# Kernel optimization log

Measured on AMD Instinct MI355X. Metric: run time of the kernel, lower is better.

The kernel has to match this reference:

```python
import jax, jax.numpy as jnp
import numpy as np

N, E, G, F_IN = 50000, 200000, 2000, 373
NEG_SLOPE, BN_EPS = 0.2, 1e-5


def _bn(x, g, b, m, v):
    # BatchNorm1d in eval mode with running stats
    return (x - m) * jax.lax.rsqrt(v + BN_EPS) * g + b


def _gcn(x, src, dst, w, b):
    # PyG GCNConv: add self loops, sym-normalize D^-1/2 (A+I) D^-1/2, then aggregate.
    n = x.shape[0]
    h = x @ w  # [N, out]
    deg = jax.ops.segment_sum(jnp.ones_like(src, jnp.float32), dst, n) + 1.0  # +1 self loop
    dinv = jax.lax.rsqrt(deg)
    agg = jax.ops.segment_sum((dinv[src] * dinv[dst])[:, None] * h[src], dst, n)
    # self-loop contribution has norm dinv[i]^2
    return agg + (dinv * dinv)[:, None] * h + b


def _gat(x, src, dst, w, a_s, a_d, b, H, C):
    # PyG GATConv (concat=True): per-edge attention logits, segment softmax over
    # incoming edges (incl. self loop, handled analytically), scatter-add aggregate.
    n = x.shape[0]
    h = (x @ w).reshape(n, H, C)  # [N, H, C]
    al_s = jnp.einsum('nhc,hc->nh', h, a_s)  # source-side logit term
    al_d = jnp.einsum('nhc,hc->nh', h, a_d)  # dest-side logit term
    e = jax.nn.leaky_relu(al_s[src] + al_d[dst], NEG_SLOPE)  # [E, H]
    e_self = jax.nn.leaky_relu(al_s + al_d, NEG_SLOPE)       # [N, H] self-loop logit
    m = jnp.maximum(jax.ops.segment_max(e, dst, n), e_self)  # stable softmax max
    we = jnp.exp(e - m[dst])
    ws = jnp.exp(e_self - m)
    denom = jax.ops.segment_sum(we, dst, n) + ws
    out = jax.ops.segment_sum(we[:, :, None] * h[src], dst, n) + ws[:, :, None] * h
    return (out / denom[:, :, None]).reshape(n, H * C) + b


def _forward(fl, edge_index, batch):
    (x, gw1, gb1, gw2, gb2, gw3, gb3,
     g01g, g01b, g01m, g01v, g02g, g02b, g02m, g02v, g03g, g03b, g03m, g03v,
     aw1, as1, ad1, ab1, aw2, as2, ad2, ab2, aw3, as3, ad3, ab3,
     g11g, g11b, g11m, g11v, g12g, g12b, g12m, g12v, g13g, g13b, g13m, g13v,
     f1w, f1b, f2w, f2b, f3w, f3b) = fl
    src, dst = edge_index[0], edge_index[1]
    xg = _bn(jax.nn.relu(_gcn(x, src, dst, gw1, gb1)), g01g, g01b, g01m, g01v)
    xg = _bn(jax.nn.relu(_gcn(xg, src, dst, gw2, gb2)), g02g, g02b, g02m, g02v)
    xg = _bn(jax.nn.relu(_gcn(xg, src, dst, gw3, gb3)), g03g, g03b, g03m, g03v)
    xg = jax.ops.segment_sum(xg, batch, G)  # global_add_pool -> [G, 128]
    y = _bn(jax.nn.relu(_gat(x, src, dst, aw1, as1, ad1, ab1, 3, 256)), g11g, g11b, g11m, g11v)
    y = _bn(jax.nn.relu(_gat(y, src, dst, aw2, as2, ad2, ab2, 3, 128)), g12g, g12b, g12m, g12v)
    y = _bn(jax.nn.relu(_gat(y, src, dst, aw3, as3, ad3, ab3, 3, 128)), g13g, g13b, g13m, g13v)
    y = jax.ops.segment_sum(y, batch, G)  # [G, 384]
    cr = jnp.concatenate([xg, y], axis=1)  # [G, 512]
    cr = jax.nn.relu(cr @ f1w + f1b)  # dropout is identity in eval mode
    cr = jax.nn.relu(cr @ f2w + f2b)
    cr = jax.nn.relu(cr @ f3w + f3b)
    return cr.reshape(-1)  # [G]


def setup_inputs() -> dict:
    key = jax.random.key(0)
    keys = jax.random.split(key, 80)
    ki = iter(range(80))
    def nrm(shape, s=0.05):
        return jax.random.normal(keys[next(ki)], shape, jnp.float32) * s
    inp = {}
    inp['x'] = jax.random.normal(keys[next(ki)], (N, F_IN), jnp.float32)
    inp['edge_index'] = jax.random.randint(keys[next(ki)], (2, E), 0, N, dtype=jnp.int32)
    inp['batch'] = jnp.sort(jax.random.randint(keys[next(ki)], (N,), 0, G, dtype=jnp.int32))
    for i, o, t in [(373, 256, '1'), (256, 128, '2'), (128, 128, '3')]:
        inp['gw' + t] = nrm((i, o))
        inp['gb' + t] = jnp.zeros((o,), jnp.float32)
    for t, d in [('01', 256), ('02', 128), ('03', 128), ('11', 768), ('12', 384), ('13', 384)]:
        inp['g' + t + 'g'] = jnp.ones((d,), jnp.float32)
        inp['g' + t + 'b'] = jnp.zeros((d,), jnp.float32)
        inp['g' + t + 'm'] = nrm((d,))
        inp['g' + t + 'v'] = jax.random.uniform(keys[next(ki)], (d,), jnp.float32) + 0.5
    for i, o, t in [(373, 256, '1'), (768, 128, '2'), (384, 128, '3')]:
        inp['aw' + t] = nrm((i, 3 * o))
        inp['as' + t] = nrm((3, o))
        inp['ad' + t] = nrm((3, o))
        inp['ab' + t] = jnp.zeros((3 * o,), jnp.float32)
    for i, o, t in [(512, 256, '1'), (256, 64, '2'), (64, 1, '3')]:
        inp['f' + t + 'w'] = nrm((i, o))
        inp['f' + t + 'b'] = jnp.zeros((o,), jnp.float32)
    return inp


def reference(x, gw1, gb1, gw2, gb2, gw3, gb3,
              g01g, g01b, g01m, g01v, g02g, g02b, g02m, g02v, g03g, g03b, g03m, g03v,
              aw1, as1, ad1, ab1, aw2, as2, ad2, ab2, aw3, as3, ad3, ab3,
              g11g, g11b, g11m, g11v, g12g, g12b, g12m, g12v, g13g, g13b, g13m, g13v,
              f1w, f1b, f2w, f2b, f3w, f3b, edge_index, batch):
    fl = (x, gw1, gb1, gw2, gb2, gw3, gb3,
          g01g, g01b, g01m, g01v, g02g, g02b, g02m, g02v, g03g, g03b, g03m, g03v,
          aw1, as1, ad1, ab1, aw2, as2, ad2, ab2, aw3, as3, ad3, ab3,
          g11g, g11b, g11m, g11v, g12g, g12b, g12m, g12v, g13g, g13b, g13m, g13v,
          f1w, f1b, f2w, f2b, f3w, f3b)
    return _forward(fl, edge_index, batch)
```

## Files before the change

### kernel.cpp

```cpp
#include <hip/hip_runtime.h>
#include <cstdint>
#include <cstddef>

#define N_NODES 50000
#define N_EDGES 200000
#define N_GRAPHS 2000
#define F_IN 373
#define NEG_SLOPE 0.2f
#define BN_EPS 1e-5f

typedef float f32x4 __attribute__((ext_vector_type(4)));
typedef float f32x2 __attribute__((ext_vector_type(2)));
typedef short s16x8 __attribute__((ext_vector_type(8)));
typedef short s16x4 __attribute__((ext_vector_type(4)));
typedef unsigned int u32x4 __attribute__((ext_vector_type(4)));

template <int VPT> struct VecT;
template <> struct VecT<2> { using type = f32x2; };
template <> struct VecT<4> { using type = f32x4; };

static inline int cdiv(long long a, long long b) { return (int)((a + b - 1) / b); }

__device__ __forceinline__ float lrelu(float x) { return x > 0.f ? x : NEG_SLOPE * x; }

__device__ __forceinline__ void atomAddF(float* p, float v) {
#if defined(__HIP_DEVICE_COMPILE__)
  unsafeAtomicAdd(p, v);
#else
  atomicAdd(p, v);
#endif
}

__device__ __forceinline__ unsigned short bf16rne(float f) {
  unsigned u = __float_as_uint(f);
  unsigned r = u + 0x7fffu + ((u >> 16) & 1u);
  return (unsigned short)(r >> 16);
}
__device__ __forceinline__ void split2(float f, unsigned short& hi, unsigned short& lo) {
  hi = bf16rne(f);
  float fh = __uint_as_float(((unsigned)hi) << 16);
  lo = bf16rne(f - fh);
}
__device__ __forceinline__ unsigned packsplit(float f) {
  unsigned short hi, lo;
  split2(f, hi, lo);
  return (((unsigned)hi) << 16) | (unsigned)lo;
}

__device__ __forceinline__ int swz(int row, int k) {
  return ((row >> 4) << 9) | ((k >> 3) << 7) | ((((row & 15) ^ (k >> 3))) << 3) | (k & 7);
}

__global__ void k_zero(float* p, long long n) {
  long long i = (long long)blockIdx.x * blockDim.x + threadIdx.x;
  if (i < n) p[i] = 0.f;
}
__global__ void k_zero_i(int* p, int n) {
  int i = blockIdx.x * blockDim.x + threadIdx.x;
  if (i < n) p[i] = 0;
}
__global__ void k_deg(int* __restrict__ deg, const int* __restrict__ dst, int e) {
  int i = blockIdx.x * blockDim.x + threadIdx.x;
  if (i < e) atomicAdd(&deg[dst[i]], 1);
}
__global__ void k_dinv(const int* __restrict__ deg, float* __restrict__ dinv, int n) {
  int i = blockIdx.x * blockDim.x + threadIdx.x;
  if (i < n) dinv[i] = rsqrtf((float)deg[i] + 1.0f);
}

__global__ void k_scan(const int* __restrict__ deg, int* __restrict__ rowptr,
                       int* __restrict__ cursor, int n) {
  __shared__ int wsum[16];
  __shared__ int carry_s;
  const int lane = threadIdx.x & 63;
  const int wid = threadIdx.x >> 6;
  if (threadIdx.x == 0) carry_s = 0;
  __syncthreads();
  for (int base = 0; base < n; base += 1024) {
    int i = base + threadIdx.x;
    int v = (i < n) ? deg[i] : 0;
    int s = v;
#pragma unroll
    for (int off = 1; off < 64; off <<= 1) {
      int t = __shfl_up(s, off);
      if (lane >= off) s += t;
    }
    if (lane == 63) wsum[wid] = s;
    __syncthreads();
    if (threadIdx.x == 0) {
      int acc = carry_s;
#pragma unroll
      for (int w = 0; w < 16; w++) { int t = wsum[w]; wsum[w] = acc; acc += t; }
      carry_s = acc;
    }
    __syncthreads();
    if (i < n) { rowptr[i] = wsum[wid] + s - v; cursor[i] = 0; }
    __syncthreads();
  }
  if (threadIdx.x == 0) rowptr[n] = carry_s;
}

__global__ void k_csr_scatter(const int* __restrict__ src, const int* __restrict__ dst,
                              const int* __restrict__ rowptr, int* __restrict__ cursor,
                              int* __restrict__ csr_src, int e) {
  int i = blockIdx.x * blockDim.x + threadIdx.x;
  if (i >= e) return;
  int d = dst[i];
  int pos = rowptr[d] + atomicAdd(&cursor[d], 1);
  csr_src[pos] = src[i];
}

__global__ void k_buildwt(const float* __restrict__ W, int ldW, int col0, int Nsub,
                          int K, int Kpad, unsigned* __restrict__ Wt) {
  int n = blockIdx.x * blockDim.x + threadIdx.x;
  int k = blockIdx.y;
  if (n >= Nsub) return;
  float v = (k < K) ? W[(size_t)k * ldW + col0 + n] : 0.f;
  Wt[(size_t)n * Kpad + k] = packsplit(v);
}

__global__ __launch_bounds__(256) void k_mfma_gemm(
    const float* __restrict__ Ap, int lda, int amode, int Kact,
    const unsigned* __restrict__ Wt, int Kpad,
    float* __restrict__ C, int M, int ldC, int col0,
    const float* __restrict__ a_s, const float* __restrict__ a_d,
    float* __restrict__ als, float* __restrict__ ald, int lshift) {
  __shared__ unsigned short Ah[64 * 32], Al[64 * 32], Bh[128 * 32], Bl[128 * 32];
  const int bm = blockIdx.y * 64;
  const int bn = blockIdx.x * 128;
  const int tid = threadIdx.x;
  const int lane = tid & 63;
  const int wave = tid >> 6;
  const int wm = wave & 1;
  const int wn = wave >> 1;

  f32x4 acc[2][4];
#pragma unroll
  for (int i = 0; i < 2; i++)
#pragma unroll
    for (int j = 0; j < 4; j++) acc[i][j] = (f32x4){0.f, 0.f, 0.f, 0.f};

  const int srow = tid >> 3;
  const int skq = (tid & 7) << 2;

  for (int k0 = 0; k0 < Kpad; k0 += 32) {
#pragma unroll
    for (int i = 0; i < 2; i++) {
      int row = i * 32 + srow;
      int grow = bm + row;
      unsigned short hv[4], lv[4];
      if (amode == 2) {
        f32x4 v = (grow < M) ? *(const f32x4*)(Ap + (size_t)grow * lda + k0 + skq)
                             : (f32x4){0.f, 0.f, 0.f, 0.f};
#pragma unroll
        for (int u = 0; u < 4; u++) split2(v[u], hv[u], lv[u]);
      } else {
        const float* ap = Ap + (size_t)grow * lda;
#pragma unroll
        for (int u = 0; u < 4; u++) {
          int kc = k0 + skq + u;
          float f = (grow < M && kc < Kact) ? ap[kc] : 0.f;
          split2(f, hv[u], lv[u]);
        }
      }
      int eb = swz(row, skq);
      *(s16x4*)&Ah[eb] = *(s16x4*)hv;
      *(s16x4*)&Al[eb] = *(s16x4*)lv;
    }
#pragma unroll
    for (int i = 0; i < 4; i++) {
      int row = i * 32 + srow;
      u32x4 v = *(const u32x4*)(Wt + (size_t)(bn + row) * Kpad + k0 + skq);
      unsigned short hv[4], lv[4];
#pragma unroll
      for (int u = 0; u < 4; u++) { hv[u] = (unsigned short)(v[u] >> 16); lv[u] = (unsigned short)(v[u] & 0xffffu); }
      int eb = swz(row, skq);
      *(s16x4*)&Bh[eb] = *(s16x4*)hv;
      *(s16x4*)&Bl[eb] = *(s16x4*)lv;
    }
    __syncthreads();
    const int koct = lane >> 4;
    const int mrow = lane & 15;
    const int fo = (koct << 7) + (((mrow ^ koct)) << 3);
    s16x8 ah[2], al[2];
#pragma unroll
    for (int g = 0; g < 2; g++) {
      int ab = ((wm * 2 + g) << 9) + fo;
      ah[g] = *(const s16x8*)&Ah[ab];
      al[g] = *(const s16x8*)&Al[ab];
    }
#pragma unroll
    for (int j = 0; j < 4; j++) {
      int bb = ((wn * 4 + j) << 9) + fo;
      s16x8 bhj = *(const s16x8*)&Bh[bb];
      s16x8 blj = *(const s16x8*)&Bl[bb];
#pragma unroll
      for (int g = 0; g < 2; g++) {
        acc[g][j] = __builtin_amdgcn_mfma_f32_16x16x32_bf16(ah[g], bhj, acc[g][j], 0, 0, 0);
        acc[g][j] = __builtin_amdgcn_mfma_f32_16x16x32_bf16(al[g], bhj, acc[g][j], 0, 0, 0);
        acc[g][j] = __builtin_amdgcn_mfma_f32_16x16x32_bf16(ah[g], blj, acc[g][j], 0, 0, 0);
      }
    }
    __syncthreads();
  }
  const int mrow = lane & 15;
  const int rq = (lane >> 4) << 2;
  float asv[4], adv[4];
  if (a_s) {
#pragma unroll
    for (int j = 0; j < 4; j++) {
      int c = bn + wn * 64 + j * 16 + mrow;
      asv[j] = a_s[c];
      adv[j] = a_d[c];
    }
  }
  const int head = bn >> lshift;
#pragma unroll
  for (int g = 0; g < 2; g++) {
#pragma unroll
    for (int r = 0; r < 4; r++) {
      int row = bm + wm * 32 + g * 16 + rq + r;
      bool rok = row < M;
      float ps = 0.f, pd = 0.f;
#pragma unroll
      for (int j = 0; j < 4; j++) {
        int ccol = bn + wn * 64 + j * 16 + mrow;
        float v = acc[g][j][r];
        if (rok) C[(size_t)row * ldC + col0 + ccol] = v;
        ps += v * asv[j];
        pd += v * adv[j];
      }
      if (a_s) {
#pragma unroll
        for (int off = 1; off < 16; off <<= 1) {
          ps += __shfl_xor(ps, off);
          pd += __shfl_xor(pd, off);
        }
        if (mrow == 0 && rok) {
          atomAddF(&als[(size_t)head * N_NODES + row], ps);
          atomAddF(&ald[(size_t)head * N_NODES + row], pd);
        }
      }
    }
  }
}

__global__ __launch_bounds__(256) void k_gemm(
    const float* __restrict__ A, const float* __restrict__ W,
    const float* __restrict__ bias, float* __restrict__ C,
    int M, int K, int Nsub, int ldW, int ldC, int col0, int flags) {
  __shared__ float As[16][68];
  __shared__ float Bs[16][68];
  const int bm = blockIdx.y * 64;
  const int bn = blockIdx.x * 64;
  const int tid = threadIdx.x;
  const int tm = (tid >> 4) << 2;
  const int tn = (tid & 15) << 2;
  float acc[4][4] = {};
  for (int k0 = 0; k0 < K; k0 += 16) {
    {
      int idx = tid * 4;
      int row = idx >> 4;
      int kk = idx & 15;
      const float* ap = A + (size_t)(bm + row) * K + k0 + kk;
      bool rok = (bm + row) < M;
#pragma unroll
      for (int i = 0; i < 4; i++) {
        int kcur = k0 + kk + i;
        As[kk + i][row] = (rok && kcur < K) ? ap[i] : 0.f;
      }
    }
#pragma unroll
    for (int i = 0; i < 4; i++) {
      int idx = tid + i * 256;
      int kk = idx >> 6;
      int nn = idx & 63;
      int kcur = k0 + kk;
      Bs[kk][nn] = (kcur < K && (bn + nn) < Nsub)
                       ? W[(size_t)kcur * ldW + col0 + bn + nn] : 0.f;
    }
    __syncthreads();
#pragma unroll
    for (int kk = 0; kk < 16; kk++) {
      float av[4], bv[4];
#pragma unroll
      for (int i = 0; i < 4; i++) av[i] = As[kk][tm + i];
#pragma unroll
      for (int j = 0; j < 4; j++) bv[j] = Bs[kk][tn + j];
#pragma unroll
      for (int i = 0; i < 4; i++)
#pragma unroll
        for (int j = 0; j < 4; j++) acc[i][j] += av[i] * bv[j];
    }
    __syncthreads();
  }
#pragma unroll
  for (int i = 0; i < 4; i++) {
    int row = bm + tm + i;
    if (row >= M) continue;
#pragma unroll
    for (int j = 0; j < 4; j++) {
      int col = bn + tn + j;
      if (col >= Nsub) continue;
      float v = acc[i][j];
      if (flags & 1) v += bias[col0 + col];
      if (flags & 2) v = fmaxf(v, 0.f);
      C[(size_t)row * ldC + col] = v;
    }
  }
}

template <int VPT>
__global__ __launch_bounds__(256) void k_gcn_fused(
    const float* __restrict__ h, const float* __restrict__ dinv,
    const int* __restrict__ rowptr, const int* __restrict__ csr_src,
    const float* __restrict__ bias, const float* __restrict__ g,
    const float* __restrict__ b, const float* __restrict__ m,
    const float* __restrict__ vv, float* __restrict__ out, int n, int F) {
  using V = typename VecT<VPT>::type;
  int wid = (blockIdx.x * blockDim.x + threadIdx.x) >> 6;
  int lane = threadIdx.x & 63;
  if (wid >= n) return;
  const int fo = lane * VPT;
  float dd = dinv[wid];
  V acc = *(const V*)(h + (size_t)wid * F + fo) * (dd * dd) + *(const V*)(bias + fo);
  int e0 = rowptr[wid], e1 = rowptr[wid + 1];
  for (int e = e0; e < e1; e++) {
    int s = csr_src[e];
    float w = dinv[s] * dd;
    acc += *(const V*)(h + (size_t)s * F + fo) * w;
  }
  V mg = *(const V*)(m + fo);
  V vg = *(const V*)(vv + fo);
  V gg = *(const V*)(g + fo);
  V bg = *(const V*)(b + fo);
  V res;
#pragma unroll
  for (int u = 0; u < VPT; u++) {
    float val = fmaxf(acc[u], 0.f);
    res[u] = (val - mg[u]) * rsqrtf(vg[u] + BN_EPS) * gg[u] + bg[u];
  }
  *(V*)(out + (size_t)wid * F + fo) = res;
}

template <int VPT>
__global__ __launch_bounds__(256) void k_gat_fused(
    const float* __restrict__ h, int ldH,
    const float* __restrict__ als, const float* __restrict__ ald,
    const int* __restrict__ rowptr, const int* __restrict__ csr_src,
    const float* __restrict__ bias, const float* __restrict__ g,
    const float* __restrict__ b, const float* __restrict__ m,
    const float* __restrict__ vv, float* __restrict__ out, int ldO, int col0, int n) {
  using V = typename VecT<VPT>::type;
  int wid = (blockIdx.x * blockDim.x + threadIdx.x) >> 6;
  int lane = threadIdx.x & 63;
  if (wid >= n) return;
  const int co = lane * VPT;
  float aldd = ald[wid];
  float self_lg = lrelu(als[wid] + aldd);
  int e0 = rowptr[wid], e1 = rowptr[wid + 1];
  float mx = self_lg;
  for (int e = e0; e < e1; e++) {
    mx = fmaxf(mx, lrelu(als[csr_src[e]] + aldd));
  }
  float den = __expf(self_lg - mx);
  V acc = *(const V*)(h + (size_t)wid * ldH + co) * den;
  for (int e = e0; e < e1; e++) {
    int s = csr_src[e];
    float w = __expf(lrelu(als[s] + aldd) - mx);
    den += w;
    acc += *(const V*)(h + (size_t)s * ldH + co) * w;
  }
  float rden = 1.f / den;
  const int fo = col0 + co;
  V bi = *(const V*)(bias + fo);
  V mg = *(const V*)(m + fo);
  V vg = *(const V*)(vv + fo);
  V gg = *(const V*)(g + fo);
  V bg = *(const V*)(b + fo);
  V res;
#pragma unroll
  for (int u = 0; u < VPT; u++) {
    float val = fmaxf(acc[u] * rden + bi[u], 0.f);
    res[u] = (val - mg[u]) * rsqrtf(vg[u] + BN_EPS) * gg[u] + bg[u];
  }
  *(V*)(out + (size_t)wid * ldO + fo) = res;
}

__global__ void k_pool_add(float* __restrict__ pooled, const float* __restrict__ act,
                           const int* __restrict__ batch, int n, int F, int off) {
  long long idx = (long long)blockIdx.x * blockDim.x + threadIdx.x;
  if (idx >= (long long)n * F) return;
  int node = (int)(idx / F);
  int f = (int)(idx % F);
  atomAddF(&pooled[(size_t)batch[node] * 512 + off + f], act[idx]);
}
__global__ void k_fc3(const float* __restrict__ in, const float* __restrict__ w,
                      const float* __restrict__ b, float* __restrict__ out, int g) {
  int wid = (blockIdx.x * blockDim.x + threadIdx.x) >> 6;
  int lane = threadIdx.x & 63;
  if (wid >= g) return;
  float v = in[wid * 64 + lane] * w[lane];
#pragma unroll
  for (int off = 32; off > 0; off >>= 1) v += __shfl_down(v, off);
  if (lane == 0) out[wid] = fmaxf(v + b[0], 0.f);
}

static void gemm_fp32(hipStream_t s, const float* A, const float* W, const float* bias,
                      float* C, int M, int K, int Nsub, int ldW, int ldC, int col0, int flags) {
  dim3 grid(cdiv(Nsub, 64), cdiv(M, 64));
  k_gemm<<<grid, 256, 0, s>>>(A, W, bias, C, M, K, Nsub, ldW, ldC, col0, flags);
}

static void gemm_mfma(hipStream_t s, const float* A, int lda, int amode,
                      const float* W, int ldW, int wcol0, int K, int Kpad,
                      unsigned* Wt, float* C, int M, int Nsub, int ldC, int ccol0,
                      const float* a_s = nullptr, const float* a_d = nullptr,
                      float* als = nullptr, float* ald = nullptr, int lshift = 30) {
  dim3 wg(cdiv(Nsub, 256), Kpad);
  k_buildwt<<<wg, 256, 0, s>>>(W, ldW, wcol0, Nsub, K, Kpad, Wt);
  dim3 grid(Nsub / 128, cdiv(M, 64));
  k_mfma_gemm<<<grid, 256, 0, s>>>(A, lda, amode, K, Wt, Kpad, C, M, ldC, ccol0,
                                   a_s, a_d, als, ald, lshift);
}

extern "C" void kernel_launch(void* const* d_in, const int* in_sizes, int n_in,
                              void* d_out, int out_size, void* d_ws, size_t ws_size,
                              hipStream_t stream) {
  const float* x = (const float*)d_in[0];
  const int* ei = (const int*)d_in[1];
  const int* batch = (const int*)d_in[2];
  const float* gw1 = (const float*)d_in[3];  const float* gb1 = (const float*)d_in[4];
  const float* gw2 = (const float*)d_in[5];  const float* gb2 = (const float*)d_in[6];
  const float* gw3 = (const float*)d_in[7];  const float* gb3 = (const float*)d_in[8];
  const float* g01g = (const float*)d_in[9];  const float* g01b = (const float*)d_in[10];
  const float* g01m = (const float*)d_in[11]; const float* g01v = (const float*)d_in[12];
  const float* g02g = (const float*)d_in[13]; const float* g02b = (const float*)d_in[14];
  const float* g02m = (const float*)d_in[15]; const float* g02v = (const float*)d_in[16];
  const float* g03g = (const float*)d_in[17]; const float* g03b = (const float*)d_in[18];
  const float* g03m = (const float*)d_in[19]; const float* g03v = (const float*)d_in[20];
  const float* g11g = (const float*)d_in[21]; const float* g11b = (const float*)d_in[22];
  const float* g11m = (const float*)d_in[23]; const float* g11v = (const float*)d_in[24];
  const float* g12g = (const float*)d_in[25]; const float* g12b = (const float*)d_in[26];
  const float* g12m = (const float*)d_in[27]; const float* g12v = (const float*)d_in[28];
  const float* g13g = (const float*)d_in[29]; const float* g13b = (const float*)d_in[30];
  const float* g13m = (const float*)d_in[31]; const float* g13v = (const float*)d_in[32];
  const float* aw1 = (const float*)d_in[33]; const float* as1 = (const float*)d_in[34];
  const float* ad1 = (const float*)d_in[35]; const float* ab1 = (const float*)d_in[36];
  const float* aw2 = (const float*)d_in[37]; const float* as2 = (const float*)d_in[38];
  const float* ad2 = (const float*)d_in[39]; const float* ad2b = nullptr;
  const float* ab2 = (const float*)d_in[40];
  const float* aw3 = (const float*)d_in[41]; const float* as3 = (const float*)d_in[42];
  const float* ad3 = (const float*)d_in[43]; const float* ab3 = (const float*)d_in[44];
  const float* f1w = (const float*)d_in[45]; const float* f1b = (const float*)d_in[46];
  const float* f2w = (const float*)d_in[47]; const float* f2b = (const float*)d_in[48];
  const float* f3w = (const float*)d_in[49]; const float* f3b = (const float*)d_in[50];
  (void)ad2b;

  const int* src = ei;
  const int* dst = ei + N_EDGES;

  size_t need = 0;
  need += (size_t)N_NODES * 768;
  need += (size_t)N_NODES * 384;
  need += (size_t)N_NODES;
  need += (size_t)N_NODES * 6;
  need += (size_t)N_NODES + 1;
  need += (size_t)N_EDGES;
  need += (size_t)N_GRAPHS * (512 + 256 + 64);
  if (ws_size < need * sizeof(float)) return;

  float* wp = (float*)d_ws;
  float* OUT = wp;     wp += (size_t)N_NODES * 768;
  float* H = wp;       wp += (size_t)N_NODES * 384;
  float* dinv = wp;    wp += N_NODES;
  float* als3 = wp;    wp += (size_t)N_NODES * 3;
  float* ald3 = wp;    wp += (size_t)N_NODES * 3;
  int* rowptr = (int*)wp;  wp += N_NODES + 1;
  int* csr_src = (int*)wp; wp += N_EDGES;
  float* pooled = wp; wp += (size_t)N_GRAPHS * 512;
  float* fc1 = wp;    wp += (size_t)N_GRAPHS * 256;
  float* fc2 = wp;    wp += (size_t)N_GRAPHS * 64;
  int* degi = (int*)als3;
  int* cursor = (int*)ald3;
  unsigned* Wt = (unsigned*)fc1;

  k_zero_i<<<cdiv(N_NODES, 256), 256, 0, stream>>>(degi, N_NODES);
  k_deg<<<cdiv(N_EDGES, 256), 256, 0, stream>>>(degi, dst, N_EDGES);
  k_dinv<<<cdiv(N_NODES, 256), 256, 0, stream>>>(degi, dinv, N_NODES);
  k_scan<<<1, 1024, 0, stream>>>(degi, rowptr, cursor, N_NODES);
  k_csr_scatter<<<cdiv(N_EDGES, 256), 256, 0, stream>>>(src, dst, rowptr, cursor, csr_src, N_EDGES);
  k_zero<<<cdiv((long long)N_GRAPHS * 512, 256), 256, 0, stream>>>(pooled, (long long)N_GRAPHS * 512);

  const int nodeWaveGrid = cdiv((long long)N_NODES * 64, 256);

  struct { const float *w, *bias, *g, *b, *m, *v; int F; } gcn[3] = {
    {gw1, gb1, g01g, g01b, g01m, g01v, 256},
    {gw2, gb2, g02g, g02b, g02m, g02v, 128},
    {gw3, gb3, g03g, g03b, g03m, g03v, 128}};
  int gF = F_IN;
  for (int l = 0; l < 3; l++) {
    int F = gcn[l].F;
    if (l == 0)
      gemm_mfma(stream, x, F_IN, 0, gcn[l].w, F, 0, F_IN, 384, Wt, H, N_NODES, F, F, 0);
    else
      gemm_mfma(stream, OUT, gF, 2, gcn[l].w, F, 0, gF, gF, Wt, H, N_NODES, F, F, 0);
    if (F == 256)
      k_gcn_fused<4><<<nodeWaveGrid, 256, 0, stream>>>(H, dinv, rowptr, csr_src,
          gcn[l].bias, gcn[l].g, gcn[l].b, gcn[l].m, gcn[l].v, OUT, N_NODES, F);
    else
      k_gcn_fused<2><<<nodeWaveGrid, 256, 0, stream>>>(H, dinv, rowptr, csr_src,
          gcn[l].bias, gcn[l].g, gcn[l].b, gcn[l].m, gcn[l].v, OUT, N_NODES, F);
    gF = F;
  }
  k_pool_add<<<cdiv((long long)N_NODES * 128, 256), 256, 0, stream>>>(pooled, OUT, batch, N_NODES, 128, 0);

  {
    int C = 256, HC = 768;
    for (int hh = 0; hh < 3; hh++) {
      k_zero<<<cdiv((long long)N_NODES * 6, 256), 256, 0, stream>>>(als3, (long long)N_NODES * 6);
      gemm_mfma(stream, x, F_IN, 0, aw1, HC, hh * C, F_IN, 384, Wt, H, N_NODES, C, C, 0,
                as1 + hh * C, ad1 + hh * C, als3, ald3, 30);
      k_gat_fused<4><<<nodeWaveGrid, 256, 0, stream>>>(H, C, als3, ald3, rowptr, csr_src,
          ab1, g11g, g11b, g11m, g11v, OUT, HC, hh * C, N_NODES);
    }
  }

  struct { const float *w, *s, *d, *bias, *g, *b, *m, *v; int K; } gat[2] = {
    {aw2, as2, ad2, ab2, g12g, g12b, g12m, g12v, 768},
    {aw3, as3, ad3, ab3, g13g, g13b, g13m, g13v, 384}};
  for (int l = 0; l < 2; l++) {
    int C = 128, HC = 384;
    k_zero<<<cdiv((long long)N_NODES * 6, 256), 256, 0, stream>>>(als3, (long long)N_NODES * 6);
    gemm_mfma(stream, OUT, gat[l].K, 2, gat[l].w, HC, 0, gat[l].K, gat[l].K, Wt, H, N_NODES, HC, HC, 0,
              gat[l].s, gat[l].d, als3, ald3, 7);
    for (int hh = 0; hh < 3; hh++) {
      k_gat_fused<2><<<nodeWaveGrid, 256, 0, stream>>>(H + hh * C, HC,
          als3 + (size_t)hh * N_NODES, ald3 + (size_t)hh * N_NODES, rowptr, csr_src,
          gat[l].bias, gat[l].g, gat[l].b, gat[l].m, gat[l].v, OUT, HC, hh * C, N_NODES);
    }
  }
  k_pool_add<<<cdiv((long long)N_NODES * 384, 256), 256, 0, stream>>>(pooled, OUT, batch, N_NODES, 384, 128);

  gemm_fp32(stream, pooled, f1w, f1b, fc1, N_GRAPHS, 512, 256, 256, 256, 0, 3);
  gemm_fp32(stream, fc1, f2w, f2b, fc2, N_GRAPHS, 256, 64, 64, 64, 0, 3);
  k_fc3<<<cdiv((long long)N_GRAPHS * 64, 256), 256, 0, stream>>>(fc2, f3w, f3b, (float*)d_out, N_GRAPHS);
}
```

Before: 1.732 ms.

## Store activations as packed bf16 hi/lo pairs and pad GEMM LDS segments

The GCN and GAT aggregation kernels now write their outputs pre-split into packed bf16 hi/lo words, so the downstream MFMA GEMM loads them with a new amode that only unpacks bits instead of redoing the float split. Pooling unpacks those words back to float. The LDS tile layout also changes from an XOR swizzle to padded 136-element segments to avoid bank conflicts. The aim is to take split arithmetic out of the GEMM A-tile load, at the cost of a small precision change in pooling and extra LDS footprint.

```diff
diff --git a/kernel.cpp b/kernel.cpp
--- a/kernel.cpp
+++ b/kernel.cpp
@@ -14,10 +14,14 @@
 typedef short s16x8 __attribute__((ext_vector_type(8)));
 typedef short s16x4 __attribute__((ext_vector_type(4)));
 typedef unsigned int u32x4 __attribute__((ext_vector_type(4)));
+typedef unsigned int u32x2 __attribute__((ext_vector_type(2)));
 
 template <int VPT> struct VecT;
 template <> struct VecT<2> { using type = f32x2; };
 template <> struct VecT<4> { using type = f32x4; };
+template <int VPT> struct UVecT;
+template <> struct UVecT<2> { using type = u32x2; };
+template <> struct UVecT<4> { using type = u32x4; };
 
 static inline int cdiv(long long a, long long b) { return (int)((a + b - 1) / b); }
 
@@ -46,9 +50,13 @@
   split2(f, hi, lo);
   return (((unsigned)hi) << 16) | (unsigned)lo;
 }
-
-__device__ __forceinline__ int swz(int row, int k) {
-  return ((row >> 4) << 9) | ((k >> 3) << 7) | ((((row & 15) ^ (k >> 3))) << 3) | (k & 7);
+__device__ __forceinline__ float unpackf(unsigned w) {
+  return __uint_as_float(w & 0xffff0000u) + __uint_as_float(w << 16);
+}
+
+#define SEGSZ 136
+__device__ __forceinline__ int ebase(int row, int k) {
+  return ((row >> 4) * 4 + (k >> 3)) * SEGSZ + ((row & 15) << 3) + (k & 7);
 }
 
 __global__ void k_zero(float* p, long long n) {
@@ -125,7 +133,8 @@
     float* __restrict__ C, int M, int ldC, int col0,
     const float* __restrict__ a_s, const float* __restrict__ a_d,
     float* __restrict__ als, float* __restrict__ ald, int lshift) {
-  __shared__ unsigned short Ah[64 * 32], Al[64 * 32], Bh[128 * 32], Bl[128 * 32];
+  __shared__ unsigned short Ah[16 * SEGSZ], Al[16 * SEGSZ];
+  __shared__ unsigned short Bh[32 * SEGSZ], Bl[32 * SEGSZ];
   const int bm = blockIdx.y * 64;
   const int bn = blockIdx.x * 128;
   const int tid = threadIdx.x;
@@ -149,7 +158,12 @@
       int row = i * 32 + srow;
       int grow = bm + row;
       unsigned short hv[4], lv[4];
-      if (amode == 2) {
+      if (amode == 1) {
+        u32x4 v = (grow < M) ? *(const u32x4*)((const unsigned*)Ap + (size_t)grow * lda + k0 + skq)
+                             : (u32x4){0u, 0u, 0u, 0u};
+#pragma unroll
+        for (int u = 0; u < 4; u++) { hv[u] = (unsigned short)(v[u] >> 16); lv[u] = (unsigned short)(v[u] & 0xffffu); }
+      } else if (amode == 2) {
         f32x4 v = (grow < M) ? *(const f32x4*)(Ap + (size_t)grow * lda + k0 + skq)
                              : (f32x4){0.f, 0.f, 0.f, 0.f};
 #pragma unroll
@@ -163,7 +177,7 @@
           split2(f, hv[u], lv[u]);
         }
       }
-      int eb = swz(row, skq);
+      int eb = ebase(row, skq);
       *(s16x4*)&Ah[eb] = *(s16x4*)hv;
       *(s16x4*)&Al[eb] = *(s16x4*)lv;
     }
@@ -174,24 +188,23 @@
       unsigned short hv[4], lv[4];
 #pragma unroll
       for (int u = 0; u < 4; u++) { hv[u] = (unsigned short)(v[u] >> 16); lv[u] = (unsigned short)(v[u] & 0xffffu); }
-      int eb = swz(row, skq);
+      int eb = ebase(row, skq);
       *(s16x4*)&Bh[eb] = *(s16x4*)hv;
       *(s16x4*)&Bl[eb] = *(s16x4*)lv;
     }
     __syncthreads();
     const int koct = lane >> 4;
     const int mrow = lane & 15;
-    const int fo = (koct << 7) + (((mrow ^ koct)) << 3);
     s16x8 ah[2], al[2];
 #pragma unroll
     for (int g = 0; g < 2; g++) {
-      int ab = ((wm * 2 + g) << 9) + fo;
+      int ab = ((wm * 2 + g) * 4 + koct) * SEGSZ + (mrow << 3);
       ah[g] = *(const s16x8*)&Ah[ab];
       al[g] = *(const s16x8*)&Al[ab];
     }
 #pragma unroll
     for (int j = 0; j < 4; j++) {
-      int bb = ((wn * 4 + j) << 9) + fo;
+      int bb = ((wn * 4 + j) * 4 + koct) * SEGSZ + (mrow << 3);
       s16x8 bhj = *(const s16x8*)&Bh[bb];
       s16x8 blj = *(const s16x8*)&Bl[bb];
 #pragma unroll
@@ -316,8 +329,9 @@
     const int* __restrict__ rowptr, const int* __restrict__ csr_src,
     const float* __restrict__ bias, const float* __restrict__ g,
     const float* __restrict__ b, const float* __restrict__ m,
-    const float* __restrict__ vv, float* __restrict__ out, int n, int F) {
+    const float* __restrict__ vv, unsigned* __restrict__ out, int n, int F) {
   using V = typename VecT<VPT>::type;
+  using UV = typename UVecT<VPT>::type;
   int wid = (blockIdx.x * blockDim.x + threadIdx.x) >> 6;
   int lane = threadIdx.x & 63;
   if (wid >= n) return;
@@ -334,13 +348,13 @@
   V vg = *(const V*)(vv + fo);
   V gg = *(const V*)(g + fo);
   V bg = *(const V*)(b + fo);
-  V res;
+  UV res;
 #pragma unroll
   for (int u = 0; u < VPT; u++) {
     float val = fmaxf(acc[u], 0.f);
-    res[u] = (val - mg[u]) * rsqrtf(vg[u] + BN_EPS) * gg[u] + bg[u];
-  }
-  *(V*)(out + (size_t)wid * F + fo) = res;
+    res[u] = packsplit((val - mg[u]) * rsqrtf(vg[u] + BN_EPS) * gg[u] + bg[u]);
+  }
+  *(UV*)(out + (size_t)wid * F + fo) = res;
 }
 
 template <int VPT>
@@ -350,8 +364,9 @@
     const int* __restrict__ rowptr, const int* __restrict__ csr_src,
     const float* __restrict__ bias, const float* __restrict__ g,
     const float* __restrict__ b, const float* __restrict__ m,
-    const float* __restrict__ vv, float* __restrict__ out, int ldO, int col0, int n) {
+    const float* __restrict__ vv, unsigned* __restrict__ out, int ldO, int col0, int n) {
   using V = typename VecT<VPT>::type;
+  using UV = typename UVecT<VPT>::type;
   int wid = (blockIdx.x * blockDim.x + threadIdx.x) >> 6;
   int lane = threadIdx.x & 63;
   if (wid >= n) return;
@@ -378,22 +393,22 @@
   V vg = *(const V*)(vv + fo);
   V gg = *(const V*)(g + fo);
   V bg = *(const V*)(b + fo);
-  V res;
+  UV res;
 #pragma unroll
   for (int u = 0; u < VPT; u++) {
     float val = fmaxf(acc[u] * rden + bi[u], 0.f);
-    res[u] = (val - mg[u]) * rsqrtf(vg[u] + BN_EPS) * gg[u] + bg[u];
-  }
-  *(V*)(out + (size_t)wid * ldO + fo) = res;
-}
-
-__global__ void k_pool_add(float* __restrict__ pooled, const float* __restrict__ act,
+    res[u] = packsplit((val - mg[u]) * rsqrtf(vg[u] + BN_EPS) * gg[u] + bg[u]);
+  }
+  *(UV*)(out + (size_t)wid * ldO + fo) = res;
+}
+
+__global__ void k_pool_add(float* __restrict__ pooled, const unsigned* __restrict__ act,
                            const int* __restrict__ batch, int n, int F, int off) {
   long long idx = (long long)blockIdx.x * blockDim.x + threadIdx.x;
   if (idx >= (long long)n * F) return;
   int node = (int)(idx / F);
   int f = (int)(idx % F);
-  atomAddF(&pooled[(size_t)batch[node] * 512 + off + f], act[idx]);
+  atomAddF(&pooled[(size_t)batch[node] * 512 + off + f], unpackf(act[idx]));
 }
 __global__ void k_fc3(const float* __restrict__ in, const float* __restrict__ w,
                       const float* __restrict__ b, float* __restrict__ out, int g) {
@@ -412,7 +427,7 @@
   k_gemm<<<grid, 256, 0, s>>>(A, W, bias, C, M, K, Nsub, ldW, ldC, col0, flags);
 }
 
-static void gemm_mfma(hipStream_t s, const float* A, int lda, int amode,
+static void gemm_mfma(hipStream_t s, const void* A, int lda, int amode,
                       const float* W, int ldW, int wcol0, int K, int Kpad,
                       unsigned* Wt, float* C, int M, int Nsub, int ldC, int ccol0,
                       const float* a_s = nullptr, const float* a_d = nullptr,
@@ -420,7 +435,7 @@
   dim3 wg(cdiv(Nsub, 256), Kpad);
   k_buildwt<<<wg, 256, 0, s>>>(W, ldW, wcol0, Nsub, K, Kpad, Wt);
   dim3 grid(Nsub / 128, cdiv(M, 64));
-  k_mfma_gemm<<<grid, 256, 0, s>>>(A, lda, amode, K, Wt, Kpad, C, M, ldC, ccol0,
+  k_mfma_gemm<<<grid, 256, 0, s>>>((const float*)A, lda, amode, K, Wt, Kpad, C, M, ldC, ccol0,
                                    a_s, a_d, als, ald, lshift);
 }
 
@@ -448,14 +463,12 @@
   const float* aw1 = (const float*)d_in[33]; const float* as1 = (const float*)d_in[34];
   const float* ad1 = (const float*)d_in[35]; const float* ab1 = (const float*)d_in[36];
   const float* aw2 = (const float*)d_in[37]; const float* as2 = (const float*)d_in[38];
-  const float* ad2 = (const float*)d_in[39]; const float* ad2b = nullptr;
-  const float* ab2 = (const float*)d_in[40];
+  const float* ad2 = (const float*)d_in[39]; const float* ab2 = (const float*)d_in[40];
   const float* aw3 = (const float*)d_in[41]; const float* as3 = (const float*)d_in[42];
   const float* ad3 = (const float*)d_in[43]; const float* ab3 = (const float*)d_in[44];
   const float* f1w = (const float*)d_in[45]; const float* f1b = (const float*)d_in[46];
   const float* f2w = (const float*)d_in[47]; const float* f2b = (const float*)d_in[48];
   const float* f3w = (const float*)d_in[49]; const float* f3b = (const float*)d_in[50];
-  (void)ad2b;
 
   const int* src = ei;
   const int* dst = ei + N_EDGES;
@@ -471,7 +484,7 @@
   if (ws_size < need * sizeof(float)) return;
 
   float* wp = (float*)d_ws;
-  float* OUT = wp;     wp += (size_t)N_NODES * 768;
+  unsigned* OUTP = (unsigned*)wp; wp += (size_t)N_NODES * 768;
   float* H = wp;       wp += (size_t)N_NODES * 384;
   float* dinv = wp;    wp += N_NODES;
   float* als3 = wp;    wp += (size_t)N_NODES * 3;
@@ -504,16 +517,16 @@
     if (l == 0)
       gemm_mfma(stream, x, F_IN, 0, gcn[l].w, F, 0, F_IN, 384, Wt, H, N_NODES, F, F, 0);
     else
-      gemm_mfma(stream, OUT, gF, 2, gcn[l].w, F, 0, gF, gF, Wt, H, N_NODES, F, F, 0);
+      gemm_mfma(stream, OUTP, gF, 1, gcn[l].w, F, 0, gF, gF, Wt, H, N_NODES, F, F, 0);
     if (F == 256)
       k_gcn_fused<4><<<nodeWaveGrid, 256, 0, stream>>>(H, dinv, rowptr, csr_src,
-          gcn[l].bias, gcn[l].g, gcn[l].b, gcn[l].m, gcn[l].v, OUT, N_NODES, F);
+          gcn[l].bias, gcn[l].g, gcn[l].b, gcn[l].m, gcn[l].v, OUTP, N_NODES, F);
     else
       k_gcn_fused<2><<<nodeWaveGrid, 256, 0, stream>>>(H, dinv, rowptr, csr_src,
-          gcn[l].bias, gcn[l].g, gcn[l].b, gcn[l].m, gcn[l].v, OUT, N_NODES, F);
+          gcn[l].bias, gcn[l].g, gcn[l].b, gcn[l].m, gcn[l].v, OUTP, N_NODES, F);
     gF = F;
   }
-  k_pool_add<<<cdiv((long long)N_NODES * 128, 256), 256, 0, stream>>>(pooled, OUT, batch, N_NODES, 128, 0);
+  k_pool_add<<<cdiv((long long)N_NODES * 128, 256), 256, 0, stream>>>(pooled, OUTP, batch, N_NODES, 128, 0);
 
   {
     int C = 256, HC = 768;
@@ -522,7 +535,7 @@
       gemm_mfma(stream, x, F_IN, 0, aw1, HC, hh * C, F_IN, 384, Wt, H, N_NODES, C, C, 0,
                 as1 + hh * C, ad1 + hh * C, als3, ald3, 30);
       k_gat_fused<4><<<nodeWaveGrid, 256, 0, stream>>>(H, C, als3, ald3, rowptr, csr_src,
-          ab1, g11g, g11b, g11m, g11v, OUT, HC, hh * C, N_NODES);
+          ab1, g11g, g11b, g11m, g11v, OUTP, HC, hh * C, N_NODES);
     }
   }
 
@@ -532,15 +545,15 @@
   for (int l = 0; l < 2; l++) {
     int C = 128, HC = 384;
     k_zero<<<cdiv((long long)N_NODES * 6, 256), 256, 0, stream>>>(als3, (long long)N_NODES * 6);
-    gemm_mfma(stream, OUT, gat[l].K, 2, gat[l].w, HC, 0, gat[l].K, gat[l].K, Wt, H, N_NODES, HC, HC, 0,
+    gemm_mfma(stream, OUTP, gat[l].K, 1, gat[l].w, HC, 0, gat[l].K, gat[l].K, Wt, H, N_NODES, HC, HC, 0,
               gat[l].s, gat[l].d, als3, ald3, 7);
     for (int hh = 0; hh < 3; hh++) {
       k_gat_fused<2><<<nodeWaveGrid, 256, 0, stream>>>(H + hh * C, HC,
           als3 + (size_t)hh * N_NODES, ald3 + (size_t)hh * N_NODES, rowptr, csr_src,
-          gat[l].bias, gat[l].g, gat[l].b, gat[l].m, gat[l].v, OUT, HC, hh * C, N_NODES);
-    }
-  }
-  k_pool_add<<<cdiv((long long)N_NODES * 384, 256), 256, 0, stream>>>(pooled, OUT, batch, N_NODES, 384, 128);
+          gat[l].bias, gat[l].g, gat[l].b, gat[l].m, gat[l].v, OUTP, HC, hh * C, N_NODES);
+    }
+  }
+  k_pool_add<<<cdiv((long long)N_NODES * 384, 256), 256, 0, stream>>>(pooled, OUTP, batch, N_NODES, 384, 128);
 
   gemm_fp32(stream, pooled, f1w, f1b, fc1, N_GRAPHS, 512, 256, 256, 256, 0, 3);
   gemm_fp32(stream, fc1, f2w, f2b, fc2, N_GRAPHS, 256, 64, 64, 64, 0, 3);
```

After: 1.748 ms. No clear change (+0.9%).
